# Kernel optimization log

Measured on AMD Instinct MI355X. Metric: run time of the kernel, lower is better.

## Reference

```python
import jax, jax.numpy as jnp
import numpy as np

GRID_SIZE = 5
SPLINE_ORDER = 3
GRID_RANGE = (-1.0, 1.0)
BATCH, IN_FEATURES, OUT_FEATURES = 8192, 512, 512


def make_grid():
    h = (GRID_RANGE[1] - GRID_RANGE[0]) / GRID_SIZE
    n = GRID_SIZE + 2 * SPLINE_ORDER + 1  # 12 knots
    return jnp.linspace(GRID_RANGE[0] - SPLINE_ORDER * h,
                        GRID_RANGE[1] + SPLINE_ORDER * h,
                        n, dtype=jnp.float32)


def b_spline(x, grid, k=SPLINE_ORDER):
    # Cox-de Boor recursion. x: (B, in) -> basis: (B, in, grid_size + k)
    x = x[..., None]                     # (B, in, 1)
    g = grid[None, None, :]              # (1, 1, n_knots)
    basis = ((x >= g[..., :-1]) & (x < g[..., 1:])).astype(x.dtype)
    for p in range(1, k + 1):
        left_denom = g[..., p:-1] - g[..., :-(p + 1)]
        right_denom = g[..., p + 1:] - g[..., 1:-p]
        left_denom = jnp.where(left_denom > 0, left_denom, jnp.ones_like(left_denom))
        right_denom = jnp.where(right_denom > 0, right_denom, jnp.ones_like(right_denom))
        left = (x - g[..., :-(p + 1)]) / left_denom * basis[..., :-1]
        right = (g[..., p + 1:] - x) / right_denom * basis[..., 1:]
        basis = left + right
    return basis


def setup_inputs() -> dict:
    key = jax.random.key(0)
    k1, k2, k3 = jax.random.split(key, 3)
    # x uniform in grid_range so spline basis is active
    x = jax.random.uniform(k1, (BATCH, IN_FEATURES), jnp.float32, minval=-1.0, maxval=1.0)
    # kaiming_uniform-like init for base weight
    bound = 1.0 / np.sqrt(IN_FEATURES)
    base_weight = jax.random.uniform(k2, (OUT_FEATURES, IN_FEATURES), jnp.float32,
                                     minval=-bound, maxval=bound)
    spline_weight = jax.random.normal(k3, (OUT_FEATURES, IN_FEATURES,
                                           GRID_SIZE + SPLINE_ORDER), jnp.float32) * 0.1
    return {"x": x, "base_weight": base_weight, "spline_weight": spline_weight}


def reference(x, base_weight, spline_weight):
    grid = make_grid()
    scale_base, scale_spline = 1.0, 1.0
    base_out = x @ base_weight.T                         # (B, out)
    basis = b_spline(x, grid, SPLINE_ORDER)              # (B, in, G+k)
    spline_out = jnp.einsum('bil,oil->bo', basis, spline_weight)
    return scale_base * base_out + scale_spline * spline_out
```

## Files before the change

### kernel.cpp

```cpp
#include <hip/hip_runtime.h>
#include <stdint.h>

typedef _Float16 half8 __attribute__((ext_vector_type(8)));
typedef float floatx4 __attribute__((ext_vector_type(4)));
typedef uint32_t u32x4 __attribute__((ext_vector_type(4)));

#define BM 128
#define BN 128
#define BK 64
#define NT 512
#define KT_BASE 8
#define KT_TOTAL 72
#define IF 512
#define NF 512
#define SW_K 4096
#define TILE_B 16384
#define WS_TILES (KT_TOTAL * 4)

__device__ __forceinline__ uint32_t swz(uint32_t b) {
  return b ^ (((b >> 7) & 7u) << 4);
}

__device__ __forceinline__ uint32_t pk(float a, float b) {
  return __builtin_bit_cast(uint32_t, __builtin_amdgcn_cvt_pkrtz(a, b));
}

__global__ __launch_bounds__(256)
void kan_prep(const float* __restrict__ bwg, const float* __restrict__ swg,
              uint32_t* __restrict__ wsB)
{
  const int gid = blockIdx.x * 256 + threadIdx.x;
  const int T = gid >> 10;
  const int q = gid & 1023;
  const int kt = T >> 2;
  const int nt = T & 3;
  const uint32_t p = swz((uint32_t)q * 16u);
  const int row = p >> 7;
  const int c   = (p & 127) >> 1;
  const int n = nt * 128 + row;
  const float* src;
  if (kt < KT_BASE) src = bwg + (size_t)n * IF   + kt * 64 + c;
  else              src = swg + (size_t)n * SW_K + (kt - KT_BASE) * 64 + c;
  float4 f0 = ((const float4*)src)[0];
  float4 f1 = ((const float4*)src)[1];
  u32x4 v; v.x = pk(f0.x, f0.y); v.y = pk(f0.z, f0.w);
           v.z = pk(f1.x, f1.y); v.w = pk(f1.z, f1.w);
  *(u32x4*)((char*)wsB + (size_t)T * TILE_B + (size_t)q * 16) = v;
}

__global__ __launch_bounds__(NT, 2)
void kan_fused(const float* __restrict__ xg, const uint32_t* __restrict__ wsB,
               float* __restrict__ outg)
{
  __shared__ _Float16 As[2][BM * BK];
  __shared__ _Float16 Bs[2][BN * BK];

  const int tid = threadIdx.x;
  const int lane = tid & 63;
  const int wv = tid >> 6;
  const int wm = wv >> 2;
  const int wn = wv & 3;

  const int bid = blockIdx.x;
  const int lb = (bid & 7) * 32 + (bid >> 3);
  const int bm0 = (lb & 63) * BM;
  const int ntI = lb >> 6;
  const int bn0 = ntI * BN;

  const int rT = tid >> 3;
  const int c8 = (tid & 7) * 8;
  const int ii = tid & 7;
  const uint32_t wA0 = swz((uint32_t)rT * 128u + (uint32_t)c8 * 2u);
  const uint32_t wA1 = swz((uint32_t)(rT + 64) * 128u + (uint32_t)c8 * 2u);

  char* AsB = (char*)As;
  char* BsB = (char*)Bs;

  uint32_t rdA[4], rdB[2];
  {
    const int rr = lane & 15;
    const uint32_t cc = (uint32_t)(lane >> 4) * 16u;
#pragma unroll
    for (int mi = 0; mi < 4; ++mi)
      rdA[mi] = swz((uint32_t)(wm * 64 + mi * 16 + rr) * 128u + cc);
#pragma unroll
    for (int ni = 0; ni < 2; ++ni)
      rdB[ni] = swz((uint32_t)(wn * 32 + ni * 16 + rr) * 128u + cc);
  }

  floatx4 acc[4][2];
#pragma unroll
  for (int mi = 0; mi < 4; ++mi)
#pragma unroll
    for (int ni = 0; ni < 2; ++ni)
      acc[mi][ni] = (floatx4){0.f, 0.f, 0.f, 0.f};

  float4 aL[4];
  float xv0, xv1;

  auto GLOADB = [&](int kt, int nb) {
    const char* src = (const char*)wsB + (size_t)(kt * 4 + ntI) * TILE_B + (size_t)tid * 16;
    char* dst = BsB + nb * TILE_B + tid * 16;
    __builtin_amdgcn_global_load_lds(
        (const __attribute__((address_space(1))) uint32_t*)src,
        (__attribute__((address_space(3))) uint32_t*)dst, 16, 0, 0);
    __builtin_amdgcn_global_load_lds(
        (const __attribute__((address_space(1))) uint32_t*)(src + 8192),
        (__attribute__((address_space(3))) uint32_t*)(dst + 8192), 16, 0, 0);
  };

  auto LOADX = [&](int kt) {
    if (kt < KT_BASE) {
      const int kb = kt * 64;
      const float* a0 = xg + (size_t)(bm0 + rT) * IF + kb + c8;
      const float* a1 = a0 + (size_t)64 * IF;
      aL[0] = ((const float4*)a0)[0]; aL[1] = ((const float4*)a0)[1];
      aL[2] = ((const float4*)a1)[0]; aL[3] = ((const float4*)a1)[1];
    } else {
      const int i0 = (kt - KT_BASE) * 8;
      xv0 = xg[(size_t)(bm0 + rT) * IF + i0 + ii];
      xv1 = xg[(size_t)(bm0 + rT + 64) * IF + i0 + ii];
    }
  };

  auto BASIS = [&](float xv) -> u32x4 {
    float u = (xv + 2.2f) * 2.5f;
    int j = (int)u;
    j = j < 3 ? 3 : (j > 7 ? 7 : j);
    float t = u - (float)j;
    float omt = 1.0f - t;
    float t2 = t * t, t3 = t2 * t;
    const float s6 = 0.16666666666666666f;
    float w0 = omt * omt * omt * s6;
    float w1 = (3.0f * t3 - 6.0f * t2 + 4.0f) * s6;
    float w2 = (-3.0f * t3 + 3.0f * t2 + 3.0f * t + 1.0f) * s6;
    float w3 = t3 * s6;
    uint32_t c0 = pk(w0, w1);
    uint32_t c1 = pk(w2, w3);
    const int j3 = j - 3;
    const bool odd = (j3 & 1) != 0;
    uint32_t lo  = odd ? (c0 << 16) : c0;
    uint32_t mid = odd ? ((c0 >> 16) | (c1 << 16)) : c1;
    uint32_t hi  = odd ? (c1 >> 16) : 0u;
    const int wofs = j3 >> 1;
    u32x4 r;
    r.x = (wofs == 0) ? lo : 0u;
    r.y = (wofs == 0) ? mid : ((wofs == 1) ? lo : 0u);
    r.z = (wofs == 0) ? hi : ((wofs == 1) ? mid : lo);
    r.w = (wofs == 1) ? hi : ((wofs == 2) ? mid : 0u);
    return r;
  };

  auto WRITEA = [&](int kt, int nb) {
    char* base = AsB + nb * TILE_B;
    if (kt < KT_BASE) {
      u32x4 v0; v0.x = pk(aL[0].x, aL[0].y); v0.y = pk(aL[0].z, aL[0].w);
                v0.z = pk(aL[1].x, aL[1].y); v0.w = pk(aL[1].z, aL[1].w);
      u32x4 v1; v1.x = pk(aL[2].x, aL[2].y); v1.y = pk(aL[2].z, aL[2].w);
                v1.z = pk(aL[3].x, aL[3].y); v1.w = pk(aL[3].z, aL[3].w);
      *(u32x4*)(base + wA0) = v0;
      *(u32x4*)(base + wA1) = v1;
    } else {
      *(u32x4*)(base + wA0) = BASIS(xv0);
      *(u32x4*)(base + wA1) = BASIS(xv1);
    }
  };

  auto COMPUTE = [&](int cb) {
    const char* ab = AsB + cb * TILE_B;
    const char* bb = BsB + cb * TILE_B;
#pragma unroll
    for (int kk = 0; kk < 2; ++kk) {
      const uint32_t ko = (uint32_t)(kk * 64);
      half8 a[4], b[2];
#pragma unroll
      for (int mi = 0; mi < 4; ++mi)
        a[mi] = *(const half8*)(ab + (rdA[mi] ^ ko));
#pragma unroll
      for (int ni = 0; ni < 2; ++ni)
        b[ni] = *(const half8*)(bb + (rdB[ni] ^ ko));
#pragma unroll
      for (int mi = 0; mi < 4; ++mi)
#pragma unroll
        for (int ni = 0; ni < 2; ++ni)
          acc[mi][ni] = __builtin_amdgcn_mfma_f32_16x16x32_f16(a[mi], b[ni], acc[mi][ni], 0, 0, 0);
    }
  };

  LOADX(0);
  GLOADB(0, 0);
  WRITEA(0, 0);
  __syncthreads();

#pragma unroll 1
  for (int kt = 0; kt < KT_TOTAL; ++kt) {
    const int cur = kt & 1;
    const int nxt = cur ^ 1;
    const bool more = (kt + 1) < KT_TOTAL;
    if (more) { GLOADB(kt + 1, nxt); LOADX(kt + 1); }
    COMPUTE(cur);
    if (more) WRITEA(kt + 1, nxt);
    __syncthreads();
  }

  const int er = (lane >> 4) * 4;
  const int ec = lane & 15;
#pragma unroll
  for (int mi = 0; mi < 4; ++mi) {
#pragma unroll
    for (int ni = 0; ni < 2; ++ni) {
      const size_t base = (size_t)(bm0 + wm * 64 + mi * 16 + er) * NF
                        + (size_t)(bn0 + wn * 32 + ni * 16 + ec);
#pragma unroll
      for (int e = 0; e < 4; ++e)
        outg[base + (size_t)e * NF] = acc[mi][ni][e];
    }
  }
}

extern "C" void kernel_launch(void* const* d_in, const int* in_sizes, int n_in,
                              void* d_out, int out_size, void* d_ws, size_t ws_size,
                              hipStream_t stream) {
  const float* x  = (const float*)d_in[0];
  const float* bw = (const float*)d_in[1];
  const float* sw = (const float*)d_in[2];
  float* out = (float*)d_out;
  uint32_t* wsB = (uint32_t*)d_ws;
  hipLaunchKernelGGL(kan_prep, dim3(WS_TILES * 1024 / 256), dim3(256), 0, stream, bw, sw, wsB);
  hipLaunchKernelGGL(kan_fused, dim3(256), dim3(NT), 0, stream, x, wsB, out);
}
```

Before: 97.09 us.

## Split K dimension in two across blocks and reduce with atomic adds

Splits the 72-step K loop into two halves handled by separate workgroups, doubling the grid from 256 to 512 blocks so more CUs are occupied. Partial sums are combined with float atomic adds into an output that a new kernel zeroes first. This trades extra launch overhead, zero-fill traffic and atomic output traffic for better machine fill.

```diff
diff --git a/kernel.cpp b/kernel.cpp
--- a/kernel.cpp
+++ b/kernel.cpp
@@ -11,6 +11,7 @@
 #define NT 512
 #define KT_BASE 8
 #define KT_TOTAL 72
+#define KT_HALF 36
 #define IF 512
 #define NF 512
 #define SW_K 4096
@@ -23,6 +24,13 @@
 
 __device__ __forceinline__ uint32_t pk(float a, float b) {
   return __builtin_bit_cast(uint32_t, __builtin_amdgcn_cvt_pkrtz(a, b));
+}
+
+__global__ __launch_bounds__(256)
+void kan_zero(float4* __restrict__ p, int n4) {
+  const int stride = gridDim.x * 256;
+  for (int i = blockIdx.x * 256 + threadIdx.x; i < n4; i += stride)
+    p[i] = (float4){0.f, 0.f, 0.f, 0.f};
 }
 
 __global__ __launch_bounds__(256)
@@ -62,10 +70,14 @@
   const int wn = wv & 3;
 
   const int bid = blockIdx.x;
-  const int lb = (bid & 7) * 32 + (bid >> 3);
+  const int u = (bid & 7) * 64 + (bid >> 3);
+  const int kz = u & 1;
+  const int lb = u >> 1;
   const int bm0 = (lb & 63) * BM;
   const int ntI = lb >> 6;
   const int bn0 = ntI * BN;
+  const int kt0 = kz * KT_HALF;
+  const int kt1 = kt0 + KT_HALF;
 
   const int rT = tid >> 3;
   const int c8 = (tid & 7) * 8;
@@ -124,10 +136,10 @@
   };
 
   auto BASIS = [&](float xv) -> u32x4 {
-    float u = (xv + 2.2f) * 2.5f;
-    int j = (int)u;
+    float u2 = (xv + 2.2f) * 2.5f;
+    int j = (int)u2;
     j = j < 3 ? 3 : (j > 7 ? 7 : j);
-    float t = u - (float)j;
+    float t = u2 - (float)j;
     float omt = 1.0f - t;
     float t2 = t * t, t3 = t2 * t;
     const float s6 = 0.16666666666666666f;
@@ -187,16 +199,16 @@
     }
   };
 
-  LOADX(0);
-  GLOADB(0, 0);
-  WRITEA(0, 0);
+  LOADX(kt0);
+  GLOADB(kt0, 0);
+  WRITEA(kt0, 0);
   __syncthreads();
 
 #pragma unroll 1
-  for (int kt = 0; kt < KT_TOTAL; ++kt) {
+  for (int kt = kt0; kt < kt1; ++kt) {
     const int cur = kt & 1;
     const int nxt = cur ^ 1;
-    const bool more = (kt + 1) < KT_TOTAL;
+    const bool more = (kt + 1) < kt1;
     if (more) { GLOADB(kt + 1, nxt); LOADX(kt + 1); }
     COMPUTE(cur);
     if (more) WRITEA(kt + 1, nxt);
@@ -213,7 +225,7 @@
                         + (size_t)(bn0 + wn * 32 + ni * 16 + ec);
 #pragma unroll
       for (int e = 0; e < 4; ++e)
-        outg[base + (size_t)e * NF] = acc[mi][ni][e];
+        unsafeAtomicAdd(outg + base + (size_t)e * NF, acc[mi][ni][e]);
     }
   }
 }
@@ -226,6 +238,7 @@
   const float* sw = (const float*)d_in[2];
   float* out = (float*)d_out;
   uint32_t* wsB = (uint32_t*)d_ws;
+  hipLaunchKernelGGL(kan_zero, dim3(2048), dim3(256), 0, stream, (float4*)out, out_size / 4);
   hipLaunchKernelGGL(kan_prep, dim3(WS_TILES * 1024 / 256), dim3(256), 0, stream, bw, sw, wsB);
-  hipLaunchKernelGGL(kan_fused, dim3(256), dim3(NT), 0, stream, x, wsB, out);
-}
+  hipLaunchKernelGGL(kan_fused, dim3(512), dim3(NT), 0, stream, x, wsB, out);
+}
```

New measurement: 88.44 us. -8.9%, faster.
